# Performance work log

Hardware: AMD Instinct MI355X
Metric: run time of the kernel (lower is better)

## Reference

```python
import jax, jax.numpy as jnp
import numpy as np

E = 1024
H = 16
D = E // H
B = 4
T = 2048


def setup_inputs() -> dict:
    key = jax.random.key(0)
    ks = jax.random.split(key, 12)
    s = 0.02
    inp = {
        "query": jax.random.normal(ks[0], (B, T, E), jnp.float32),
        "key_in": jax.random.normal(ks[1], (B, T, E), jnp.float32),
        "value": jax.random.normal(ks[2], (B, T, E), jnp.float32),
        "mask": jnp.tril(jnp.ones((T, T), jnp.int32))[None, None, :, :],
        "Wq": jax.random.normal(ks[3], (E, E), jnp.float32) * s,
        "bq": jnp.zeros((E,), jnp.float32),
        "Wk": jax.random.normal(ks[4], (E, E), jnp.float32) * s,
        "bk": jnp.zeros((E,), jnp.float32),
        "Wv": jax.random.normal(ks[5], (E, E), jnp.float32) * s,
        "bv": jnp.zeros((E,), jnp.float32),
        "Wo": jax.random.normal(ks[6], (E, E), jnp.float32) * s,
        "bo": jnp.zeros((E,), jnp.float32),
    }
    return inp


def _shape(x):
    # [B, T, E] -> [B, H, T, D]
    return x.reshape(B, -1, H, D).transpose(0, 2, 1, 3)


def reference(query, key_in, value, mask, Wq, bq, Wk, bk, Wv, bv, Wo, bo):
    q = _shape(query @ Wq.T + bq)
    k = _shape(key_in @ Wk.T + bk)
    v = _shape(value @ Wv.T + bv)
    scale = 1.0 / jnp.sqrt(jnp.float32(D))
    # [B, H, Tq, Tk]
    scores = jnp.einsum("bhqd,bhkd->bhqk", q, k) * scale
    scores = jnp.where(mask == 0, jnp.float32(-jnp.inf), scores)
    attn = jax.nn.softmax(scores, axis=-1)
    out = jnp.einsum("bhqk,bhkd->bhqd", attn, v)
    out = out.transpose(0, 2, 1, 3).reshape(B, T, E)
    return out @ Wo.T + bo
```

## Files before the change

### kernel.cpp

```cpp
#include <hip/hip_runtime.h>
#include <hip/hip_bf16.h>
#include <cstdint>

#define BB 4
#define TT 2048
#define EE 1024
#define HH 16
#define DD 64
#define BH (BB*HH)
#define MM (BB*TT)
#define KK 1024
#define KSTR 72
#define VSTR 136
#define LOG2E 1.44269504088896340736f

typedef __attribute__((ext_vector_type(8))) short short8;
typedef __attribute__((ext_vector_type(4))) short short4_;
typedef __attribute__((ext_vector_type(4))) float float4_;
typedef __attribute__((ext_vector_type(4))) ushort ushort4_;

__device__ __forceinline__ void gl_lds16(const void* g, void* l) {
    __builtin_amdgcn_global_load_lds(
        (const __attribute__((address_space(1))) void*)g,
        (__attribute__((address_space(3))) void*)l, 16, 0, 0);
}

__device__ __forceinline__ ushort f2bf(float v) {
    __hip_bfloat16 h = __float2bfloat16(v);
    return *(ushort*)&h;
}

__global__ __launch_bounds__(256) void cvt_kernel(
    const float* __restrict__ s0, ushort* __restrict__ d0, int n0,
    const float* __restrict__ s1, ushort* __restrict__ d1, int n1,
    const float* __restrict__ s2, ushort* __restrict__ d2, int n2,
    const float* __restrict__ s3, ushort* __restrict__ d3, int n3)
{
    const float* s; ushort* d; int n;
    switch (blockIdx.y) {
        case 0: s = s0; d = d0; n = n0; break;
        case 1: s = s1; d = d1; n = n1; break;
        case 2: s = s2; d = d2; n = n2; break;
        default: s = s3; d = d3; n = n3; break;
    }
    int i = (blockIdx.x * 256 + threadIdx.x) * 4;
    if (i >= n) return;
    float4_ v = *(const float4_*)&s[i];
    ushort4_ o;
#pragma unroll
    for (int j = 0; j < 4; j++) o[j] = f2bf(v[j]);
    *(ushort4_*)&d[i] = o;
}

__global__ __launch_bounds__(256, 3) void gemm_qkv(
    const float* __restrict__ Aq, const float* __restrict__ Ak,
    const float* __restrict__ Av,
    const ushort* __restrict__ Wqc, const ushort* __restrict__ Wkc,
    const ushort* __restrict__ Wvc,
    const float* __restrict__ bq, const float* __restrict__ bk,
    const float* __restrict__ bv,
    ushort* __restrict__ Oq, ushort* __restrict__ Ok, ushort* __restrict__ Ov,
    float qscale)
{
    __shared__ __align__(16) float  Asf[128*32];
    __shared__ __align__(16) ushort Bs [128*32];

    const int bid = blockIdx.x;
    const int swz = (bid & 7) * 192 + (bid >> 3);
    const int z   = swz >> 9;
    const int rem = swz & 511;
    const int bx  = rem & 7;
    const int by  = rem >> 3;

    const float*  A    = (z == 0) ? Aq  : (z == 1) ? Ak  : Av;
    const ushort* W    = (z == 0) ? Wqc : (z == 1) ? Wkc : Wvc;
    const float*  bias = (z == 0) ? bq  : (z == 1) ? bk  : bv;
    ushort*       Cout = (z == 0) ? Oq  : (z == 1) ? Ok  : Ov;
    const float   scale = (z == 0) ? qscale : 1.0f;
    const bool    modeT = (z == 2);

    const int tid  = threadIdx.x;
    const int wave = tid >> 6;
    const int lane = tid & 63;
    const int l15  = lane & 15;
    const int quad = lane >> 4;
    const int wm   = wave & 1;
    const int wn   = wave >> 1;

    const long rowBase = (long)by * 128;
    const long colBase = (long)bx * 128;

    float4_ acc[4][4];
#pragma unroll
    for (int i = 0; i < 4; i++)
#pragma unroll
        for (int j = 0; j < 4; j++) acc[i][j] = float4_{0.f, 0.f, 0.f, 0.f};

    for (int k0 = 0; k0 < KK; k0 += 32) {
        __syncthreads();
#pragma unroll
        for (int it = 0; it < 4; it++) {
            int idx = it * 256 + tid;
            int r = idx >> 3, c4 = (idx & 7) * 4;
            gl_lds16(A + (rowBase + r) * KK + k0 + c4, &Asf[idx * 4]);
        }
#pragma unroll
        for (int it = 0; it < 2; it++) {
            int idx = it * 256 + tid;
            int r = idx >> 2, c8 = (idx & 3) * 8;
            gl_lds16(W + (colBase + r) * KK + k0 + c8, &Bs[idx * 8]);
        }
        __syncthreads();

        short8 af[4], bf[4];
#pragma unroll
        for (int mt = 0; mt < 4; mt++) {
            const float* arow = &Asf[(wm*64 + mt*16 + l15) * 32 + quad*8];
            float4_ a0 = *(const float4_*)&arow[0];
            float4_ a1 = *(const float4_*)&arow[4];
#pragma unroll
            for (int j = 0; j < 4; j++) {
                af[mt][j]     = (short)f2bf(a0[j]);
                af[mt][j + 4] = (short)f2bf(a1[j]);
            }
        }
#pragma unroll
        for (int nt = 0; nt < 4; nt++)
            bf[nt] = *(const short8*)&Bs[(wn*64 + nt*16 + l15) * 32 + quad*8];
#pragma unroll
        for (int mt = 0; mt < 4; mt++)
#pragma unroll
            for (int nt = 0; nt < 4; nt++)
                acc[mt][nt] = __builtin_amdgcn_mfma_f32_16x16x32_bf16(
                    af[mt], bf[nt], acc[mt][nt], 0, 0, 0);
    }

#pragma unroll
    for (int nt = 0; nt < 4; nt++) {
        const long col = colBase + wn*64 + nt*16 + l15;
        const float bvv = bias[col];
        const long h = col >> 6, d = col & (DD - 1);
#pragma unroll
        for (int mt = 0; mt < 4; mt++) {
            const long row0 = rowBase + wm*64 + mt*16 + quad*4;
            if (modeT) {
                const long b = row0 >> 11, t0 = row0 & (TT - 1);
                ushort4_ pk;
#pragma unroll
                for (int i = 0; i < 4; i++) pk[i] = f2bf((acc[mt][nt][i] + bvv) * scale);
                *(ushort4_*)&Cout[((b*HH + h)*DD + d)*TT + t0] = pk;
            } else {
#pragma unroll
                for (int i = 0; i < 4; i++) {
                    const long row = row0 + i;
                    const long b = row >> 11, t = row & (TT - 1);
                    Cout[(((b*HH + h) * TT) + t) * DD + d] =
                        f2bf((acc[mt][nt][i] + bvv) * scale);
                }
            }
        }
    }
}

__global__ __launch_bounds__(256, 3) void gemm_out(
    const ushort* __restrict__ A, const ushort* __restrict__ W,
    const float* __restrict__ bias, float* __restrict__ Cout)
{
    __shared__ __align__(16) ushort As[128*32];
    __shared__ __align__(16) ushort Bs[128*32];

    const int bid = blockIdx.x;
    const int swz = (bid & 7) * 64 + (bid >> 3);
    const int bx  = swz & 7;
    const int by  = swz >> 3;

    const int tid  = threadIdx.x;
    const int wave = tid >> 6;
    const int lane = tid & 63;
    const int l15  = lane & 15;
    const int quad = lane >> 4;
    const int wm   = wave & 1;
    const int wn   = wave >> 1;

    const long rowBase = (long)by * 128;
    const long colBase = (long)bx * 128;

    float4_ acc[4][4];
#pragma unroll
    for (int i = 0; i < 4; i++)
#pragma unroll
        for (int j = 0; j < 4; j++) acc[i][j] = float4_{0.f, 0.f, 0.f, 0.f};

    for (int k0 = 0; k0 < KK; k0 += 32) {
        __syncthreads();
#pragma unroll
        for (int it = 0; it < 2; it++) {
            int idx = it * 256 + tid;
            int r   = idx >> 2;
            int c8  = (idx & 3) * 8;
            gl_lds16(A + (rowBase + r) * KK + k0 + c8, &As[idx * 8]);
            gl_lds16(W + (colBase + r) * KK + k0 + c8, &Bs[idx * 8]);
        }
        __syncthreads();

        short8 af[4], bf[4];
#pragma unroll
        for (int mt = 0; mt < 4; mt++)
            af[mt] = *(const short8*)&As[(wm*64 + mt*16 + l15) * 32 + quad*8];
#pragma unroll
        for (int nt = 0; nt < 4; nt++)
            bf[nt] = *(const short8*)&Bs[(wn*64 + nt*16 + l15) * 32 + quad*8];
#pragma unroll
        for (int mt = 0; mt < 4; mt++)
#pragma unroll
            for (int nt = 0; nt < 4; nt++)
                acc[mt][nt] = __builtin_amdgcn_mfma_f32_16x16x32_bf16(
                    af[mt], bf[nt], acc[mt][nt], 0, 0, 0);
    }

#pragma unroll
    for (int nt = 0; nt < 4; nt++) {
        const long col = colBase + wn*64 + nt*16 + l15;
        const float bv = bias[col];
#pragma unroll
        for (int mt = 0; mt < 4; mt++) {
            const long row0 = rowBase + wm*64 + mt*16 + quad*4;
#pragma unroll
            for (int i = 0; i < 4; i++)
                Cout[(row0 + i) * EE + col] = acc[mt][nt][i] + bv;
        }
    }
}

__global__ __launch_bounds__(512, 4) void flash_kernel(
    const ushort* __restrict__ Qh, const ushort* __restrict__ Kh,
    const ushort* __restrict__ Vt, ushort* __restrict__ AO)
{
    __shared__ __align__(16) ushort Ks[128*KSTR];
    __shared__ __align__(16) ushort Vs[64*VSTR];

    const int qt  = (TT/128 - 1) - blockIdx.x;
    const int bh  = blockIdx.y;
    const int tid = threadIdx.x;
    const int wave = tid >> 6, lane = tid & 63;
    const int l15 = lane & 15, quad = lane >> 4;

    const ushort* Qb = Qh + (long)bh * TT * DD;
    const ushort* Kb = Kh + (long)bh * TT * DD;
    const ushort* Vb = Vt + (long)bh * DD * TT;

    const int qrow = qt*128 + wave*16 + l15;
    short8 aq0 = *(const short8*)&Qb[(long)qrow * DD + quad*8];
    short8 aq1 = *(const short8*)&Qb[(long)qrow * DD + 32 + quad*8];

    float4_ o[4];
#pragma unroll
    for (int nt = 0; nt < 4; nt++) o[nt] = float4_{0.f, 0.f, 0.f, 0.f};
    float m_run = -INFINITY, l_run = 0.0f;

    const int nkt = qt + 1;

    short8 kreg[2], vreg[2];
#pragma unroll
    for (int it = 0; it < 2; it++) {
        int c = it * 512 + tid;
        int kk = c >> 3, ks = c & 7;
        kreg[it] = *(const short8*)&Kb[(long)kk * DD + ks*8];
        int dd = c >> 4, vs = c & 15;
        vreg[it] = *(const short8*)&Vb[(long)dd * TT + vs*8];
    }

    for (int kt = 0; kt < nkt; kt++) {
        __syncthreads();
#pragma unroll
        for (int it = 0; it < 2; it++) {
            int c = it * 512 + tid;
            int kk = c >> 3, ks = c & 7;
            *(short8*)&Ks[kk*KSTR + ks*8] = kreg[it];
            int dd = c >> 4, vs = c & 15;
            *(short8*)&Vs[dd*VSTR + vs*8] = vreg[it];
        }
        __syncthreads();

        if (kt + 1 < nkt) {
            const long koff = (long)(kt+1) * 128;
#pragma unroll
            for (int it = 0; it < 2; it++) {
                int c = it * 512 + tid;
                int kk = c >> 3, ks = c & 7;
                kreg[it] = *(const short8*)&Kb[(koff + kk) * DD + ks*8];
                int dd = c >> 4, vs = c & 15;
                vreg[it] = *(const short8*)&Vb[(long)dd * TT + koff + vs*8];
            }
        }

        float4_ s[8];
        __builtin_amdgcn_s_setprio(1);
#pragma unroll
        for (int nt = 0; nt < 8; nt++) {
            short8 bk0 = *(const short8*)&Ks[(nt*16 + l15) * KSTR + quad*8];
            short8 bk1 = *(const short8*)&Ks[(nt*16 + l15) * KSTR + 32 + quad*8];
            float4_ acc = float4_{0.f, 0.f, 0.f, 0.f};
            acc = __builtin_amdgcn_mfma_f32_16x16x32_bf16(bk0, aq0, acc, 0,0,0);
            acc = __builtin_amdgcn_mfma_f32_16x16x32_bf16(bk1, aq1, acc, 0,0,0);
            s[nt] = acc;
        }
        __builtin_amdgcn_s_setprio(0);

        if (kt == nkt - 1) {
#pragma unroll
            for (int nt = 0; nt < 8; nt++) {
#pragma unroll
                for (int i = 0; i < 4; i++) {
                    const int key = kt*128 + nt*16 + quad*4 + i;
                    if (key > qrow) s[nt][i] = -INFINITY;
                }
            }
        }

        float t8[8];
#pragma unroll
        for (int nt = 0; nt < 8; nt++)
            t8[nt] = fmaxf(fmaxf(s[nt][0], s[nt][1]), fmaxf(s[nt][2], s[nt][3]));
        float pm = fmaxf(fmaxf(fmaxf(t8[0], t8[1]), fmaxf(t8[2], t8[3])),
                         fmaxf(fmaxf(t8[4], t8[5]), fmaxf(t8[6], t8[7])));
        pm = fmaxf(pm, __shfl_xor(pm, 16));
        pm = fmaxf(pm, __shfl_xor(pm, 32));

        if (!__all(pm <= m_run + 8.0f)) {
            const float mnew = fmaxf(m_run, pm);
            const float alpha = exp2f(m_run - mnew);
            m_run = mnew;
            l_run *= alpha;
#pragma unroll
            for (int nt = 0; nt < 4; nt++)
#pragma unroll
                for (int i = 0; i < 4; i++) o[nt][i] *= alpha;
        }

        float rs0 = 0.f, rs1 = 0.f, rs2 = 0.f, rs3 = 0.f;
        short8 pb[4];
#pragma unroll
        for (int c = 0; c < 4; c++) {
#pragma unroll
            for (int half = 0; half < 2; half++) {
                const int nt = 2*c + half;
                const float p0 = exp2f(s[nt][0] - m_run);
                const float p1 = exp2f(s[nt][1] - m_run);
                const float p2 = exp2f(s[nt][2] - m_run);
                const float p3 = exp2f(s[nt][3] - m_run);
                rs0 += p0; rs1 += p1; rs2 += p2; rs3 += p3;
                pb[c][half*4 + 0] = (short)f2bf(p0);
                pb[c][half*4 + 1] = (short)f2bf(p1);
                pb[c][half*4 + 2] = (short)f2bf(p2);
                pb[c][half*4 + 3] = (short)f2bf(p3);
            }
        }
        float rs = (rs0 + rs1) + (rs2 + rs3);
        rs += __shfl_xor(rs, 16);
        rs += __shfl_xor(rs, 32);
        l_run += rs;

        __builtin_amdgcn_s_setprio(1);
#pragma unroll
        for (int c = 0; c < 4; c++) {
            const short8 bp = pb[c];
#pragma unroll
            for (int nt = 0; nt < 4; nt++) {
                const ushort* vrow = &Vs[(nt*16 + l15) * VSTR];
                short4_ lo = *(const short4_*)&vrow[(2*c    )*16 + quad*4];
                short4_ hi = *(const short4_*)&vrow[(2*c + 1)*16 + quad*4];
                short8 av;
                av[0]=lo[0]; av[1]=lo[1]; av[2]=lo[2]; av[3]=lo[3];
                av[4]=hi[0]; av[5]=hi[1]; av[6]=hi[2]; av[7]=hi[3];
                o[nt] = __builtin_amdgcn_mfma_f32_16x16x32_bf16(av, bp, o[nt], 0,0,0);
            }
        }
        __builtin_amdgcn_s_setprio(0);
    }

    const int h = bh & (HH - 1);
    const int b = bh >> 4;
    const float inv = 1.0f / l_run;
    const long rowOff = ((long)(b*TT + qrow)) * EE + h*64;
#pragma unroll
    for (int nt = 0; nt < 4; nt++) {
        ushort4_ pk;
#pragma unroll
        for (int i = 0; i < 4; i++) pk[i] = f2bf(o[nt][i] * inv);
        *(ushort4_*)&AO[rowOff + nt*16 + quad*4] = pk;
    }
}

extern "C" void kernel_launch(void* const* d_in, const int* in_sizes, int n_in,
                              void* d_out, int out_size, void* d_ws, size_t ws_size,
                              hipStream_t stream)
{
    const float* query  = (const float*)d_in[0];
    const float* key_in = (const float*)d_in[1];
    const float* value  = (const float*)d_in[2];
    const float* Wq = (const float*)d_in[4];
    const float* bq = (const float*)d_in[5];
    const float* Wk = (const float*)d_in[6];
    const float* bk = (const float*)d_in[7];
    const float* Wv = (const float*)d_in[8];
    const float* bv = (const float*)d_in[9];
    const float* Wo = (const float*)d_in[10];
    const float* bo = (const float*)d_in[11];

    ushort* ws = (ushort*)d_ws;
    const size_t NIN = (size_t)MM * KK;
    const size_t NW  = (size_t)EE * KK;
    ushort* Wqc = ws;
    ushort* Wkc = Wqc + NW;
    ushort* Wvc = Wkc + NW;
    ushort* Woc = Wvc + NW;
    ushort* Qh  = Woc + NW;
    ushort* Kh  = Qh + NIN;
    ushort* Vth = Kh + NIN;
    ushort* AO  = Vth + NIN;

    const dim3 cvtW_grid(NW/1024, 4);

    cvt_kernel<<<cvtW_grid, 256, 0, stream>>>(Wq, Wqc, (int)NW, Wk, Wkc, (int)NW,
                                              Wv, Wvc, (int)NW, Wo, Woc, (int)NW);

    gemm_qkv<<<dim3(3 * (EE/128) * (MM/128)), 256, 0, stream>>>(
        query, key_in, value, Wqc, Wkc, Wvc, bq, bk, bv, Qh, Kh, Vth,
        0.125f * LOG2E);

    flash_kernel<<<dim3(TT/128, BH), 512, 0, stream>>>(Qh, Kh, Vth, AO);

    gemm_out<<<dim3((EE/128) * (MM/128)), 256, 0, stream>>>(AO, Woc, bo, (float*)d_out);
}
```

Baseline: 416.1 us.

## Pair causal query tiles per block and double-buffer K/V in LDS

Each flash-attention block now processes two query tiles, a long one (15-p) and a short one (p). This balances the causal work per block and halves the grid. The K/V shared-memory tiles are double-buffered so the next tile is written to the alternate buffer after compute, which drops one barrier per iteration. In exchange, LDS use doubles, which may lower occupancy, and the grid has fewer blocks to spread across CUs.

```diff
diff --git a/kernel.cpp b/kernel.cpp
--- a/kernel.cpp
+++ b/kernel.cpp
@@ -236,10 +236,10 @@
     const ushort* __restrict__ Qh, const ushort* __restrict__ Kh,
     const ushort* __restrict__ Vt, ushort* __restrict__ AO)
 {
-    __shared__ __align__(16) ushort Ks[128*KSTR];
-    __shared__ __align__(16) ushort Vs[64*VSTR];
-
-    const int qt  = (TT/128 - 1) - blockIdx.x;
+    __shared__ __align__(16) ushort Ks[2][128*KSTR];
+    __shared__ __align__(16) ushort Vs[2][64*VSTR];
+
+    const int p   = blockIdx.x;
     const int bh  = blockIdx.y;
     const int tid = threadIdx.x;
     const int wave = tid >> 6, lane = tid & 63;
@@ -248,147 +248,162 @@
     const ushort* Qb = Qh + (long)bh * TT * DD;
     const ushort* Kb = Kh + (long)bh * TT * DD;
     const ushort* Vb = Vt + (long)bh * DD * TT;
-
-    const int qrow = qt*128 + wave*16 + l15;
-    short8 aq0 = *(const short8*)&Qb[(long)qrow * DD + quad*8];
-    short8 aq1 = *(const short8*)&Qb[(long)qrow * DD + 32 + quad*8];
-
-    float4_ o[4];
-#pragma unroll
-    for (int nt = 0; nt < 4; nt++) o[nt] = float4_{0.f, 0.f, 0.f, 0.f};
-    float m_run = -INFINITY, l_run = 0.0f;
-
-    const int nkt = qt + 1;
-
-    short8 kreg[2], vreg[2];
+    const int h = bh & (HH - 1);
+    const int b = bh >> 4;
+
+    int kks[2], kss[2], dds[2], vss[2];
 #pragma unroll
     for (int it = 0; it < 2; it++) {
         int c = it * 512 + tid;
-        int kk = c >> 3, ks = c & 7;
-        kreg[it] = *(const short8*)&Kb[(long)kk * DD + ks*8];
-        int dd = c >> 4, vs = c & 15;
-        vreg[it] = *(const short8*)&Vb[(long)dd * TT + vs*8];
-    }
-
-    for (int kt = 0; kt < nkt; kt++) {
-        __syncthreads();
+        kks[it] = c >> 3; kss[it] = c & 7;
+        dds[it] = c >> 4; vss[it] = c & 15;
+    }
+
+#pragma unroll
+    for (int seg = 0; seg < 2; seg++) {
+        const int qt  = (seg == 0) ? (15 - p) : p;
+        const int nkt = qt + 1;
+
+        const int qrow = qt*128 + wave*16 + l15;
+        short8 aq0 = *(const short8*)&Qb[(long)qrow * DD + quad*8];
+        short8 aq1 = *(const short8*)&Qb[(long)qrow * DD + 32 + quad*8];
+
+        float4_ o[4];
+#pragma unroll
+        for (int nt = 0; nt < 4; nt++) o[nt] = float4_{0.f, 0.f, 0.f, 0.f};
+        float m_run = -INFINITY, l_run = 0.0f;
+
+        short8 kreg[2], vreg[2];
 #pragma unroll
         for (int it = 0; it < 2; it++) {
-            int c = it * 512 + tid;
-            int kk = c >> 3, ks = c & 7;
-            *(short8*)&Ks[kk*KSTR + ks*8] = kreg[it];
-            int dd = c >> 4, vs = c & 15;
-            *(short8*)&Vs[dd*VSTR + vs*8] = vreg[it];
-        }
-        __syncthreads();
-
-        if (kt + 1 < nkt) {
-            const long koff = (long)(kt+1) * 128;
-#pragma unroll
-            for (int it = 0; it < 2; it++) {
-                int c = it * 512 + tid;
-                int kk = c >> 3, ks = c & 7;
-                kreg[it] = *(const short8*)&Kb[(koff + kk) * DD + ks*8];
-                int dd = c >> 4, vs = c & 15;
-                vreg[it] = *(const short8*)&Vb[(long)dd * TT + koff + vs*8];
-            }
-        }
-
-        float4_ s[8];
-        __builtin_amdgcn_s_setprio(1);
-#pragma unroll
-        for (int nt = 0; nt < 8; nt++) {
-            short8 bk0 = *(const short8*)&Ks[(nt*16 + l15) * KSTR + quad*8];
-            short8 bk1 = *(const short8*)&Ks[(nt*16 + l15) * KSTR + 32 + quad*8];
-            float4_ acc = float4_{0.f, 0.f, 0.f, 0.f};
-            acc = __builtin_amdgcn_mfma_f32_16x16x32_bf16(bk0, aq0, acc, 0,0,0);
-            acc = __builtin_amdgcn_mfma_f32_16x16x32_bf16(bk1, aq1, acc, 0,0,0);
-            s[nt] = acc;
-        }
-        __builtin_amdgcn_s_setprio(0);
-
-        if (kt == nkt - 1) {
+            kreg[it] = *(const short8*)&Kb[(long)kks[it] * DD + kss[it]*8];
+            vreg[it] = *(const short8*)&Vb[(long)dds[it] * TT + vss[it]*8];
+        }
+        __syncthreads();
+#pragma unroll
+        for (int it = 0; it < 2; it++) {
+            *(short8*)&Ks[0][kks[it]*KSTR + kss[it]*8] = kreg[it];
+            *(short8*)&Vs[0][dds[it]*VSTR + vss[it]*8] = vreg[it];
+        }
+        __syncthreads();
+        int cur = 0;
+
+        for (int kt = 0; kt < nkt; kt++) {
+            if (kt + 1 < nkt) {
+                const long koff = (long)(kt+1) * 128;
+#pragma unroll
+                for (int it = 0; it < 2; it++) {
+                    kreg[it] = *(const short8*)&Kb[(koff + kks[it]) * DD + kss[it]*8];
+                    vreg[it] = *(const short8*)&Vb[(long)dds[it] * TT + koff + vss[it]*8];
+                }
+            }
+            const ushort* ksb = &Ks[cur][0];
+            const ushort* vsb = &Vs[cur][0];
+
+            float4_ s[8];
+            __builtin_amdgcn_s_setprio(1);
 #pragma unroll
             for (int nt = 0; nt < 8; nt++) {
-#pragma unroll
-                for (int i = 0; i < 4; i++) {
-                    const int key = kt*128 + nt*16 + quad*4 + i;
-                    if (key > qrow) s[nt][i] = -INFINITY;
-                }
-            }
-        }
-
-        float t8[8];
-#pragma unroll
-        for (int nt = 0; nt < 8; nt++)
-            t8[nt] = fmaxf(fmaxf(s[nt][0], s[nt][1]), fmaxf(s[nt][2], s[nt][3]));
-        float pm = fmaxf(fmaxf(fmaxf(t8[0], t8[1]), fmaxf(t8[2], t8[3])),
-                         fmaxf(fmaxf(t8[4], t8[5]), fmaxf(t8[6], t8[7])));
-        pm = fmaxf(pm, __shfl_xor(pm, 16));
-        pm = fmaxf(pm, __shfl_xor(pm, 32));
-
-        if (!__all(pm <= m_run + 8.0f)) {
-            const float mnew = fmaxf(m_run, pm);
-            const float alpha = exp2f(m_run - mnew);
-            m_run = mnew;
-            l_run *= alpha;
-#pragma unroll
-            for (int nt = 0; nt < 4; nt++)
-#pragma unroll
-                for (int i = 0; i < 4; i++) o[nt][i] *= alpha;
-        }
-
-        float rs0 = 0.f, rs1 = 0.f, rs2 = 0.f, rs3 = 0.f;
-        short8 pb[4];
-#pragma unroll
-        for (int c = 0; c < 4; c++) {
-#pragma unroll
-            for (int half = 0; half < 2; half++) {
-                const int nt = 2*c + half;
-                const float p0 = exp2f(s[nt][0] - m_run);
-                const float p1 = exp2f(s[nt][1] - m_run);
-                const float p2 = exp2f(s[nt][2] - m_run);
-                const float p3 = exp2f(s[nt][3] - m_run);
-                rs0 += p0; rs1 += p1; rs2 += p2; rs3 += p3;
-                pb[c][half*4 + 0] = (short)f2bf(p0);
-                pb[c][half*4 + 1] = (short)f2bf(p1);
-                pb[c][half*4 + 2] = (short)f2bf(p2);
-                pb[c][half*4 + 3] = (short)f2bf(p3);
-            }
-        }
-        float rs = (rs0 + rs1) + (rs2 + rs3);
-        rs += __shfl_xor(rs, 16);
-        rs += __shfl_xor(rs, 32);
-        l_run += rs;
-
-        __builtin_amdgcn_s_setprio(1);
-#pragma unroll
-        for (int c = 0; c < 4; c++) {
-            const short8 bp = pb[c];
-#pragma unroll
-            for (int nt = 0; nt < 4; nt++) {
-                const ushort* vrow = &Vs[(nt*16 + l15) * VSTR];
-                short4_ lo = *(const short4_*)&vrow[(2*c    )*16 + quad*4];
-                short4_ hi = *(const short4_*)&vrow[(2*c + 1)*16 + quad*4];
-                short8 av;
-                av[0]=lo[0]; av[1]=lo[1]; av[2]=lo[2]; av[3]=lo[3];
-                av[4]=hi[0]; av[5]=hi[1]; av[6]=hi[2]; av[7]=hi[3];
-                o[nt] = __builtin_amdgcn_mfma_f32_16x16x32_bf16(av, bp, o[nt], 0,0,0);
-            }
-        }
-        __builtin_amdgcn_s_setprio(0);
-    }
-
-    const int h = bh & (HH - 1);
-    const int b = bh >> 4;
-    const float inv = 1.0f / l_run;
-    const long rowOff = ((long)(b*TT + qrow)) * EE + h*64;
-#pragma unroll
-    for (int nt = 0; nt < 4; nt++) {
-        ushort4_ pk;
-#pragma unroll
-        for (int i = 0; i < 4; i++) pk[i] = f2bf(o[nt][i] * inv);
-        *(ushort4_*)&AO[rowOff + nt*16 + quad*4] = pk;
+                short8 bk0 = *(const short8*)&ksb[(nt*16 + l15) * KSTR + quad*8];
+                short8 bk1 = *(const short8*)&ksb[(nt*16 + l15) * KSTR + 32 + quad*8];
+                float4_ acc = float4_{0.f, 0.f, 0.f, 0.f};
+                acc = __builtin_amdgcn_mfma_f32_16x16x32_bf16(bk0, aq0, acc, 0,0,0);
+                acc = __builtin_amdgcn_mfma_f32_16x16x32_bf16(bk1, aq1, acc, 0,0,0);
+                s[nt] = acc;
+            }
+            __builtin_amdgcn_s_setprio(0);
+
+            if (kt == nkt - 1) {
+#pragma unroll
+                for (int nt = 0; nt < 8; nt++) {
+#pragma unroll
+                    for (int i = 0; i < 4; i++) {
+                        const int key = kt*128 + nt*16 + quad*4 + i;
+                        if (key > qrow) s[nt][i] = -INFINITY;
+                    }
+                }
+            }
+
+            float t8[8];
+#pragma unroll
+            for (int nt = 0; nt < 8; nt++)
+                t8[nt] = fmaxf(fmaxf(s[nt][0], s[nt][1]), fmaxf(s[nt][2], s[nt][3]));
+            float pm = fmaxf(fmaxf(fmaxf(t8[0], t8[1]), fmaxf(t8[2], t8[3])),
+                             fmaxf(fmaxf(t8[4], t8[5]), fmaxf(t8[6], t8[7])));
+            pm = fmaxf(pm, __shfl_xor(pm, 16));
+            pm = fmaxf(pm, __shfl_xor(pm, 32));
+
+            if (!__all(pm <= m_run + 8.0f)) {
+                const float mnew = fmaxf(m_run, pm);
+                const float alpha = exp2f(m_run - mnew);
+                m_run = mnew;
+                l_run *= alpha;
+#pragma unroll
+                for (int nt = 0; nt < 4; nt++)
+#pragma unroll
+                    for (int i = 0; i < 4; i++) o[nt][i] *= alpha;
+            }
+
+            float rs0 = 0.f, rs1 = 0.f, rs2 = 0.f, rs3 = 0.f;
+            short8 pb[4];
+#pragma unroll
+            for (int c = 0; c < 4; c++) {
+#pragma unroll
+                for (int half = 0; half < 2; half++) {
+                    const int nt = 2*c + half;
+                    const float p0 = exp2f(s[nt][0] - m_run);
+                    const float p1 = exp2f(s[nt][1] - m_run);
+                    const float p2 = exp2f(s[nt][2] - m_run);
+                    const float p3 = exp2f(s[nt][3] - m_run);
+                    rs0 += p0; rs1 += p1; rs2 += p2; rs3 += p3;
+                    pb[c][half*4 + 0] = (short)f2bf(p0);
+                    pb[c][half*4 + 1] = (short)f2bf(p1);
+                    pb[c][half*4 + 2] = (short)f2bf(p2);
+                    pb[c][half*4 + 3] = (short)f2bf(p3);
+                }
+            }
+            float rs = (rs0 + rs1) + (rs2 + rs3);
+            rs += __shfl_xor(rs, 16);
+            rs += __shfl_xor(rs, 32);
+            l_run += rs;
+
+            __builtin_amdgcn_s_setprio(1);
+#pragma unroll
+            for (int c = 0; c < 4; c++) {
+                const short8 bp = pb[c];
+#pragma unroll
+                for (int nt = 0; nt < 4; nt++) {
+                    const ushort* vrow = &vsb[(nt*16 + l15) * VSTR];
+                    short4_ lo = *(const short4_*)&vrow[(2*c    )*16 + quad*4];
+                    short4_ hi = *(const short4_*)&vrow[(2*c + 1)*16 + quad*4];
+                    short8 av;
+                    av[0]=lo[0]; av[1]=lo[1]; av[2]=lo[2]; av[3]=lo[3];
+                    av[4]=hi[0]; av[5]=hi[1]; av[6]=hi[2]; av[7]=hi[3];
+                    o[nt] = __builtin_amdgcn_mfma_f32_16x16x32_bf16(av, bp, o[nt], 0,0,0);
+                }
+            }
+            __builtin_amdgcn_s_setprio(0);
+
+            if (kt + 1 < nkt) {
+#pragma unroll
+                for (int it = 0; it < 2; it++) {
+                    *(short8*)&Ks[cur^1][kks[it]*KSTR + kss[it]*8] = kreg[it];
+                    *(short8*)&Vs[cur^1][dds[it]*VSTR + vss[it]*8] = vreg[it];
+                }
+                __syncthreads();
+                cur ^= 1;
+            }
+        }
+
+        const float inv = 1.0f / l_run;
+        const long rowOff = ((long)(b*TT + qrow)) * EE + h*64;
+#pragma unroll
+        for (int nt = 0; nt < 4; nt++) {
+            ushort4_ pk;
+#pragma unroll
+            for (int i = 0; i < 4; i++) pk[i] = f2bf(o[nt][i] * inv);
+            *(ushort4_*)&AO[rowOff + nt*16 + quad*4] = pk;
+        }
     }
 }
 
@@ -429,7 +444,7 @@
         query, key_in, value, Wqc, Wkc, Wvc, bq, bk, bv, Qh, Kh, Vth,
         0.125f * LOG2E);
 
-    flash_kernel<<<dim3(TT/128, BH), 512, 0, stream>>>(Qh, Kh, Vth, AO);
+    flash_kernel<<<dim3(8, BH), 512, 0, stream>>>(Qh, Kh, Vth, AO);
 
     gemm_out<<<dim3((EE/128) * (MM/128)), 256, 0, stream>>>(AO, Woc, bo, (float*)d_out);
 }
```

After: 364.7 us. 12.4% less time.
